# Kernel optimization log

Hardware: AMD Instinct MI355X
Metric: run time of the kernel (lower is better)

Reference implementation:

```python
import jax, jax.numpy as jnp
import numpy as np

B, T, H, NH = 2, 2048, 1024, 16
HD = H // NH


def setup_inputs() -> dict:
    key = jax.random.key(0)
    ks = jax.random.split(key, 12)
    s = 1.0 / np.sqrt(H)
    inp = {
        "q": jax.random.normal(ks[0], (B, T, H), jnp.float32),
        "k": jax.random.normal(ks[1], (B, T, H), jnp.float32),
        "v": jax.random.normal(ks[2], (B, T, H), jnp.float32),
        "mask": jnp.tril(jnp.ones((T, T), jnp.int32))[None, None],  # causal [1,1,T,T]
        "w_q": jax.random.normal(ks[3], (H, H), jnp.float32) * s,
        "b_q": jax.random.normal(ks[4], (H,), jnp.float32) * 0.01,
        "w_k": jax.random.normal(ks[5], (H, H), jnp.float32) * s,
        "b_k": jax.random.normal(ks[6], (H,), jnp.float32) * 0.01,
        "w_v": jax.random.normal(ks[7], (H, H), jnp.float32) * s,
        "b_v": jax.random.normal(ks[8], (H,), jnp.float32) * 0.01,
        "w_o": jax.random.normal(ks[9], (H, H), jnp.float32) * s,
        "b_o": jax.random.normal(ks[10], (H,), jnp.float32) * 0.01,
    }
    return inp


def reference(q, k, v, mask, w_q, b_q, w_k, b_k, w_v, b_v, w_o, b_o):
    def split_heads(x):
        Bx, Tx, _ = x.shape
        return x.reshape(Bx, Tx, NH, HD).transpose(0, 2, 1, 3)  # [B,NH,T,HD]

    Q = split_heads(q @ w_q.T + b_q)
    K = split_heads(k @ w_k.T + b_k)
    V = split_heads(v @ w_v.T + b_v)

    scores = jnp.einsum("bhqd,bhkd->bhqk", Q, K) / np.sqrt(HD).astype(np.float32)
    scores = jnp.where(mask == 0, jnp.float32(-1e9), scores)
    weights = jax.nn.softmax(scores, axis=-1)  # dropout prob = 0.0
    out = jnp.einsum("bhqk,bhkd->bhqd", weights, V)
    out = out.transpose(0, 2, 1, 3).reshape(q.shape[0], q.shape[1], H)
    return out @ w_o.T + b_o
```

## Files before the change

### kernel.cpp

```cpp
#include <hip/hip_runtime.h>
#include <hip/hip_bf16.h>

#define Bb 2
#define Tt 2048
#define Hh 1024
#define NHh 16

typedef short bf16x8 __attribute__((ext_vector_type(8)));
typedef float f32x4 __attribute__((ext_vector_type(4)));
typedef unsigned short u16;
typedef unsigned int u32;
typedef u16 u16x4v __attribute__((ext_vector_type(4)));
typedef u32 u32x2v __attribute__((ext_vector_type(2)));

#define QK_SCALE 0.180336880f

#if __has_builtin(__builtin_amdgcn_exp2f)
__device__ __forceinline__ float exp2_fast(float x) { return __builtin_amdgcn_exp2f(x); }
#else
__device__ __forceinline__ float exp2_fast(float x) { return __expf(x * 0.69314718f); }
#endif

__device__ __forceinline__ u16 f2b(float x) {
  unsigned u = __builtin_bit_cast(unsigned, x);
  u += 0x7FFFu + ((u >> 16) & 1u);
  return (u16)(u >> 16);
}
__device__ __forceinline__ float b2f(u16 x) {
  return __builtin_bit_cast(float, (u32)x << 16);
}

__device__ __forceinline__ u32 cvt_pk(float lo, float hi) {
  u32 r;
  asm("v_cvt_pk_bf16_f32 %0, %1, %2" : "=v"(r) : "v"(lo), "v"(hi));
  return r;
}

__global__ __launch_bounds__(256) void cvt_all_kernel(
    const float* __restrict__ q, const float* __restrict__ k, const float* __restrict__ v,
    const float* __restrict__ wq, const float* __restrict__ wk,
    const float* __restrict__ wv, const float* __restrict__ wo,
    u16* __restrict__ qb, u16* __restrict__ kb, u16* __restrict__ vb,
    u16* __restrict__ wqb, u16* __restrict__ wkb, u16* __restrict__ wvb,
    u16* __restrict__ wob, int n4_in, int n4_w) {
  const int which = blockIdx.y;
  const float* src;
  u16* dst;
  int n4;
  float sc = 1.0f;
  switch (which) {
    case 0: src = q;  dst = qb;  n4 = n4_in; break;
    case 1: src = k;  dst = kb;  n4 = n4_in; break;
    case 2: src = v;  dst = vb;  n4 = n4_in; break;
    case 3: src = wq; dst = wqb; n4 = n4_w; sc = QK_SCALE; break;
    case 4: src = wk; dst = wkb; n4 = n4_w; break;
    case 5: src = wv; dst = wvb; n4 = n4_w; break;
    default: src = wo; dst = wob; n4 = n4_w; break;
  }
  int i = blockIdx.x * blockDim.x + threadIdx.x;
  int stride = gridDim.x * blockDim.x;
  for (; i < n4; i += stride) {
    float4 vv = ((const float4*)src)[i];
    u16x4v o;
    o.x = f2b(vv.x * sc); o.y = f2b(vv.y * sc); o.z = f2b(vv.z * sc); o.w = f2b(vv.w * sc);
    ((u16x4v*)dst)[i] = o;
  }
}

template<int NF, int MODE>
__device__ __forceinline__ void gemm_body(const u16* __restrict__ A,
                                          const u16* __restrict__ W,
                                          const float* __restrict__ bias, float bscale,
                                          void* __restrict__ Cout,
                                          u16* lA, u16* lB, int mt, int nt) {
  const int tid = threadIdx.x;
  const int lane = tid & 63;
  const int wid = tid >> 6;
  const int wr = wid >> 1, wc = wid & 1;
  const int g = lane >> 4, fr = lane & 15;
  constexpr int NT = NF * 32;

  f32x4 acc[4][NF];
#pragma unroll
  for (int m = 0; m < 4; ++m)
#pragma unroll
    for (int n = 0; n < NF; ++n) acc[m][n] = (f32x4){0.f, 0.f, 0.f, 0.f};

  const int srow = tid >> 3;
  const int scol = (tid & 7) * 8;

  bf16x8 ra[4], rb[NF];
#pragma unroll
  for (int ps = 0; ps < 4; ++ps)
    ra[ps] = *(const bf16x8*)(A + (size_t)(mt * 128 + ps * 32 + srow) * Hh + scol);
#pragma unroll
  for (int ps = 0; ps < NF; ++ps)
    rb[ps] = *(const bf16x8*)(W + (size_t)(nt * NT + ps * 32 + srow) * Hh + scol);
#pragma unroll
  for (int ps = 0; ps < 4; ++ps) {
    int r = ps * 32 + srow;
    *(bf16x8*)((char*)lA + r * 128 + ((scol * 2) ^ ((r & 7) << 4))) = ra[ps];
  }
#pragma unroll
  for (int ps = 0; ps < NF; ++ps) {
    int r = ps * 32 + srow;
    *(bf16x8*)((char*)lB + r * 128 + ((scol * 2) ^ ((r & 7) << 4))) = rb[ps];
  }
  __syncthreads();

  for (int kt = 0; kt < Hh; kt += 64) {
    if (kt + 64 < Hh) {
#pragma unroll
      for (int ps = 0; ps < 4; ++ps)
        ra[ps] = *(const bf16x8*)(A + (size_t)(mt * 128 + ps * 32 + srow) * Hh + kt + 64 + scol);
#pragma unroll
      for (int ps = 0; ps < NF; ++ps)
        rb[ps] = *(const bf16x8*)(W + (size_t)(nt * NT + ps * 32 + srow) * Hh + kt + 64 + scol);
    }
    bf16x8 af[4][2], bfv[NF][2];
#pragma unroll
    for (int m = 0; m < 4; ++m)
#pragma unroll
      for (int ks = 0; ks < 2; ++ks) {
        int r = wr * 64 + m * 16 + fr;
        af[m][ks] = *(const bf16x8*)((const char*)lA + r * 128 + ((ks * 64 + g * 16) ^ ((r & 7) << 4)));
      }
#pragma unroll
    for (int n = 0; n < NF; ++n)
#pragma unroll
      for (int ks = 0; ks < 2; ++ks) {
        int r = wc * (NT / 2) + n * 16 + fr;
        bfv[n][ks] = *(const bf16x8*)((const char*)lB + r * 128 + ((ks * 64 + g * 16) ^ ((r & 7) << 4)));
      }
#pragma unroll
    for (int m = 0; m < 4; ++m)
#pragma unroll
      for (int n = 0; n < NF; ++n)
#pragma unroll
        for (int ks = 0; ks < 2; ++ks)
          acc[m][n] = __builtin_amdgcn_mfma_f32_16x16x32_bf16(af[m][ks], bfv[n][ks],
                                                              acc[m][n], 0, 0, 0);
    if (kt + 64 < Hh) {
      __syncthreads();
#pragma unroll
      for (int ps = 0; ps < 4; ++ps) {
        int r = ps * 32 + srow;
        *(bf16x8*)((char*)lA + r * 128 + ((scol * 2) ^ ((r & 7) << 4))) = ra[ps];
      }
#pragma unroll
      for (int ps = 0; ps < NF; ++ps) {
        int r = ps * 32 + srow;
        *(bf16x8*)((char*)lB + r * 128 + ((scol * 2) ^ ((r & 7) << 4))) = rb[ps];
      }
      __syncthreads();
    }
  }

#pragma unroll
  for (int n = 0; n < NF; ++n) {
    int Cc = nt * NT + wc * (NT / 2) + n * 16 + fr;
    float bv = bias[Cc] * bscale;
#pragma unroll
    for (int m = 0; m < 4; ++m) {
#pragma unroll
      for (int j = 0; j < 4; ++j) {
        int R = mt * 128 + wr * 64 + m * 16 + g * 4 + j;
        float val = acc[m][n][j] + bv;
        if constexpr (MODE == 0) {
          int bb = R >> 11, t = R & (Tt - 1);
          int h = Cc >> 6, d = Cc & 63;
          ((u16*)Cout)[(((size_t)(bb * NHh + h) * Tt + t) << 6) + d] = f2b(val);
        } else if constexpr (MODE == 2) {
          int bb = R >> 11, t = R & (Tt - 1);
          int h = Cc >> 6, d = Cc & 63;
          ((u16*)Cout)[(((size_t)(bb * NHh + h) * 64 + d) << 11) + t] = f2b(val);
        } else {
          ((float*)Cout)[(size_t)R * Hh + Cc] = val;
        }
      }
    }
  }
}

__global__ __launch_bounds__(256, 3) void proj_qkv_kernel(
    const u16* __restrict__ qb, const u16* __restrict__ kb, const u16* __restrict__ vb,
    const u16* __restrict__ wqb, const u16* __restrict__ wkb, const u16* __restrict__ wvb,
    const float* __restrict__ biq, const float* __restrict__ bik, const float* __restrict__ biv,
    u16* __restrict__ Qp, u16* __restrict__ Kp, u16* __restrict__ Vt) {
  __shared__ u16 lA[128 * 64];
  __shared__ u16 lB[128 * 64];
  const int id = blockIdx.x;
  const int nt = (id >> 3) & 7;
  const int slot = (id & 7) + 8 * (id >> 6);
  const int z = slot >> 5, mt = slot & 31;
  if (z == 0)      gemm_body<4, 0>(qb, wqb, biq, QK_SCALE, Qp, lA, lB, mt, nt);
  else if (z == 1) gemm_body<4, 0>(kb, wkb, bik, 1.0f, Kp, lA, lB, mt, nt);
  else             gemm_body<4, 2>(vb, wvb, biv, 1.0f, Vt, lA, lB, mt, nt);
}

__global__ __launch_bounds__(256, 2) void gemm_out_kernel(
    const u16* __restrict__ A, const u16* __restrict__ W,
    const float* __restrict__ bias, float* __restrict__ Cout) {
  __shared__ u16 lA[128 * 64];
  __shared__ u16 lB[64 * 64];
  const int id = blockIdx.x;
  const int j = id >> 3;
  const int mt = (id & 7) + 8 * (j >> 4);
  const int nt = j & 15;
  gemm_body<2, 1>(A, W, bias, 1.0f, Cout, lA, lB, mt, nt);
}

__global__ __launch_bounds__(256, 4) void attn_kernel(const u16* __restrict__ Qp,
                                                      const u16* __restrict__ Kp,
                                                      const u16* __restrict__ Vt,
                                                      u16* __restrict__ AO,
                                                      u16* __restrict__ Obuf,
                                                      float2* __restrict__ MLbuf) {
  __shared__ u16 lK[2][64 * 64];
  __shared__ u16 lV[2][64 * 64];
  __shared__ u16 lP[64 * 64];
  const int tid = threadIdx.x;
  const int lane = tid & 63;
  const int w = tid >> 6;
  const int g = lane >> 4, fr = lane & 15;

  const int id = blockIdx.x;
  int bh, qt, kv0, kv1, chunk = 0;
  bool split;
  if (id < 512) {
    bh = id & 31; qt = 16 + (id >> 5);
    kv0 = 0; kv1 = 15; split = true;
  } else {
    int r = id - 512;
    int d = 16 - (r >> 6);
    int p = r & 63;
    bh = p & 31;
    if (p < 32) { qt = d - 1;  kv0 = 0;  kv1 = qt; split = false; }
    else        { qt = 15 + d; kv0 = 16; kv1 = qt; split = true; chunk = 1; }
  }
  const int q0 = qt * 64;

  bf16x8 qf[2];
  {
    const u16* qrow = Qp + (((size_t)bh * Tt + q0 + w * 16 + fr) << 6) + g * 8;
    qf[0] = *(const bf16x8*)(qrow);
    qf[1] = *(const bf16x8*)(qrow + 32);
  }

  const int srow = tid >> 3;
  const int scol = (tid & 7) * 8;
  const int sswz = (scol * 2) ^ ((srow & 7) << 4);

  bf16x8 rk[2], rv[2];
#pragma unroll
  for (int ps = 0; ps < 2; ++ps) {
    rk[ps] = *(const bf16x8*)(Kp + (((size_t)bh * Tt + kv0 * 64 + ps * 32 + srow) << 6) + scol);
    rv[ps] = *(const bf16x8*)(Vt + (((size_t)bh * 64 + ps * 32 + srow) << 11) + kv0 * 64 + scol);
  }
#pragma unroll
  for (int ps = 0; ps < 2; ++ps) {
    *(bf16x8*)((char*)lK[0] + (ps * 32 + srow) * 128 + sswz) = rk[ps];
    *(bf16x8*)((char*)lV[0] + (ps * 32 + srow) * 128 + sswz) = rv[ps];
  }
  __syncthreads();

  float m_r = -1e30f, l_r = 0.f;
  f32x4 acc[4];
#pragma unroll
  for (int nd = 0; nd < 4; ++nd) acc[nd] = (f32x4){0.f, 0.f, 0.f, 0.f};

  const int prow = w * 16 + fr;
  const int psw = (prow & 7) << 4;
  const int qoff = w * 16 + fr;

  for (int jt = kv0; jt <= kv1; ++jt) {
    const char* bK = (const char*)lK[jt & 1];
    const char* bV = (const char*)lV[jt & 1];
    if (jt < kv1) {
#pragma unroll
      for (int ps = 0; ps < 2; ++ps) {
        rk[ps] = *(const bf16x8*)(Kp + (((size_t)bh * Tt + (jt + 1) * 64 + ps * 32 + srow) << 6) + scol);
        rv[ps] = *(const bf16x8*)(Vt + (((size_t)bh * 64 + ps * 32 + srow) << 11) + (jt + 1) * 64 + scol);
      }
    }
    f32x4 s[4];
    __builtin_amdgcn_s_setprio(1);
#pragma unroll
    for (int n = 0; n < 4; ++n) {
      s[n] = (f32x4){0.f, 0.f, 0.f, 0.f};
      int rbase = (n * 16 + fr) * 128;
      int rsw = (fr & 7) << 4;
#pragma unroll
      for (int ks = 0; ks < 2; ++ks) {
        bf16x8 ak = *(const bf16x8*)(bK + rbase + ((ks * 64 + g * 16) ^ rsw));
        s[n] = __builtin_amdgcn_mfma_f32_16x16x32_bf16(ak, qf[ks], s[n], 0, 0, 0);
      }
    }
    __builtin_amdgcn_s_setprio(0);

    float tm = -1e30f;
    if (jt == qt) {
#pragma unroll
      for (int n = 0; n < 4; ++n)
#pragma unroll
        for (int r = 0; r < 4; ++r) {
          if (n * 16 + g * 4 + r > qoff) s[n][r] = -1e30f;
          tm = fmaxf(tm, s[n][r]);
        }
    } else {
#pragma unroll
      for (int n = 0; n < 4; ++n)
#pragma unroll
        for (int r = 0; r < 4; ++r) tm = fmaxf(tm, s[n][r]);
    }
    tm = fmaxf(tm, __shfl_xor(tm, 16));
    tm = fmaxf(tm, __shfl_xor(tm, 32));
    if (!__all(tm <= m_r + 8.0f)) {
      float mn = fmaxf(m_r, tm);
      float sc = exp2_fast(m_r - mn);
      m_r = mn;
      l_r *= sc;
      float scj[4];
#pragma unroll
      for (int j = 0; j < 4; ++j) scj[j] = __shfl(sc, g * 4 + j);
#pragma unroll
      for (int nd = 0; nd < 4; ++nd)
#pragma unroll
        for (int j = 0; j < 4; ++j) acc[nd][j] *= scj[j];
    }
    float rs = 0.f;
    u32 pw[4][2];
#pragma unroll
    for (int n = 0; n < 4; ++n) {
      float p0 = exp2_fast(s[n][0] - m_r);
      float p1 = exp2_fast(s[n][1] - m_r);
      float p2 = exp2_fast(s[n][2] - m_r);
      float p3 = exp2_fast(s[n][3] - m_r);
      rs += (p0 + p1) + (p2 + p3);
      pw[n][0] = cvt_pk(p0, p1);
      pw[n][1] = cvt_pk(p2, p3);
    }
    rs += __shfl_xor(rs, 16);
    rs += __shfl_xor(rs, 32);
    l_r += rs;
    bf16x8 pa[2];
    {
      char* base = (char*)lP + prow * 128;
#pragma unroll
      for (int n = 0; n < 4; ++n)
        *(u32x2v*)(base + ((32 * n + 8 * g) ^ psw)) = (u32x2v){pw[n][0], pw[n][1]};
#pragma unroll
      for (int ks = 0; ks < 2; ++ks)
        pa[ks] = *(const bf16x8*)(base + ((ks * 64 + g * 16) ^ psw));
    }
    __builtin_amdgcn_s_setprio(1);
#pragma unroll
    for (int nd = 0; nd < 4; ++nd) {
      int rbase = (nd * 16 + fr) * 128;
      int rsw = (fr & 7) << 4;
#pragma unroll
      for (int ks = 0; ks < 2; ++ks) {
        bf16x8 bv = *(const bf16x8*)(bV + rbase + ((ks * 64 + g * 16) ^ rsw));
        acc[nd] = __builtin_amdgcn_mfma_f32_16x16x32_bf16(pa[ks], bv, acc[nd], 0, 0, 0);
      }
    }
    __builtin_amdgcn_s_setprio(0);
    if (jt < kv1) {
#pragma unroll
      for (int ps = 0; ps < 2; ++ps) {
        *(bf16x8*)((char*)lK[(jt + 1) & 1] + (ps * 32 + srow) * 128 + sswz) = rk[ps];
        *(bf16x8*)((char*)lV[(jt + 1) & 1] + (ps * 32 + srow) * 128 + sswz) = rv[ps];
      }
      __syncthreads();
    }
  }

  if (!split) {
    const int b = bh >> 4, hh = bh & 15;
    float lj[4];
#pragma unroll
    for (int j = 0; j < 4; ++j) lj[j] = __shfl(l_r, g * 4 + j);
#pragma unroll
    for (int j = 0; j < 4; ++j) {
      float inv = 1.0f / lj[j];
      int qq = q0 + w * 16 + g * 4 + j;
      size_t base = (((size_t)b * Tt + qq) << 10) + hh * 64;
#pragma unroll
      for (int nd = 0; nd < 4; ++nd)
        AO[base + nd * 16 + fr] = f2b(acc[nd][j] * inv);
    }
  } else {
    const int pidx = ((bh * 16 + (qt - 16)) << 1) + chunk;
    if (g == 0) MLbuf[pidx * 64 + w * 16 + fr] = make_float2(m_r, l_r);
    u16* ob = Obuf + (size_t)pidx * 4096;
#pragma unroll
    for (int j = 0; j < 4; ++j) {
      int row = w * 16 + g * 4 + j;
#pragma unroll
      for (int nd = 0; nd < 4; ++nd)
        ob[row * 64 + nd * 16 + fr] = f2b(acc[nd][j]);
    }
  }
}

__global__ __launch_bounds__(256) void merge_kernel(const u16* __restrict__ Obuf,
                                                    const float2* __restrict__ MLbuf,
                                                    u16* __restrict__ AO) {
  const int row_id = blockIdx.x * 256 + threadIdx.x;
  const int bh = row_id >> 10;
  const int qs = (row_id >> 6) & 15;
  const int row = row_id & 63;
  const int tile = bh * 16 + qs;
  float2 ml0 = MLbuf[(tile * 2 + 0) * 64 + row];
  float2 ml1 = MLbuf[(tile * 2 + 1) * 64 + row];
  float M = fmaxf(ml0.x, ml1.x);
  float w0 = exp2_fast(ml0.x - M);
  float w1 = exp2_fast(ml1.x - M);
  float inv = 1.0f / (w0 * ml0.y + w1 * ml1.y);
  const u16* o0 = Obuf + (size_t)(tile * 2 + 0) * 4096 + row * 64;
  const u16* o1 = Obuf + (size_t)(tile * 2 + 1) * 4096 + row * 64;
  const int qt = 16 + qs;
  const int qq = qt * 64 + row;
  const int b = bh >> 4, hh = bh & 15;
  u16* dst = AO + (((size_t)b * Tt + qq) << 10) + hh * 64;
#pragma unroll
  for (int c = 0; c < 8; ++c) {
    bf16x8 v0 = *(const bf16x8*)(o0 + c * 8);
    bf16x8 v1 = *(const bf16x8*)(o1 + c * 8);
    bf16x8 o;
#pragma unroll
    for (int e = 0; e < 8; ++e)
      o[e] = (short)f2b((w0 * b2f((u16)v0[e]) + w1 * b2f((u16)v1[e])) * inv);
    *(bf16x8*)(dst + c * 8) = o;
  }
}

extern "C" void kernel_launch(void* const* d_in, const int* in_sizes, int n_in,
                              void* d_out, int out_size, void* d_ws, size_t ws_size,
                              hipStream_t stream) {
  const float* q   = (const float*)d_in[0];
  const float* k   = (const float*)d_in[1];
  const float* v   = (const float*)d_in[2];
  const float* wq  = (const float*)d_in[4];
  const float* bq  = (const float*)d_in[5];
  const float* wk  = (const float*)d_in[6];
  const float* bk  = (const float*)d_in[7];
  const float* wv  = (const float*)d_in[8];
  const float* bv  = (const float*)d_in[9];
  const float* wo  = (const float*)d_in[10];
  const float* bo  = (const float*)d_in[11];

  char* ws = (char*)d_ws;
  const size_t SZB = (size_t)Bb * Tt * Hh * 2;
  const size_t WB  = (size_t)Hh * Hh * 2;
  u16* qb  = (u16*)(ws);
  u16* kb  = (u16*)(ws + SZB);
  u16* vb  = (u16*)(ws + 2 * SZB);
  u16* wqb = (u16*)(ws + 3 * SZB);
  u16* wkb = (u16*)(ws + 3 * SZB + WB);
  u16* wvb = (u16*)(ws + 3 * SZB + 2 * WB);
  u16* wob = (u16*)(ws + 3 * SZB + 3 * WB);
  u16* Qp  = (u16*)(ws + 3 * SZB + 4 * WB);
  u16* Kp  = (u16*)(ws + 4 * SZB + 4 * WB);
  u16* Vt  = (u16*)(ws + 5 * SZB + 4 * WB);
  u16* AO  = qb;
  u16* Obuf = kb;
  float2* MLbuf = (float2*)vb;

  const int N4_IN = (Bb * Tt * Hh) / 4;
  const int N4_W  = (Hh * Hh) / 4;
  cvt_all_kernel<<<dim3(512, 7), 256, 0, stream>>>(
      q, k, v, wq, wk, wv, wo, qb, kb, vb, wqb, wkb, wvb, wob, N4_IN, N4_W);

  proj_qkv_kernel<<<dim3(768), 256, 0, stream>>>(
      qb, kb, vb, wqb, wkb, wvb, bq, bk, bv, Qp, Kp, Vt);

  attn_kernel<<<dim3(1536), 256, 0, stream>>>(Qp, Kp, Vt, AO, Obuf, MLbuf);

  merge_kernel<<<dim3(128), 256, 0, stream>>>(Obuf, MLbuf, AO);

  gemm_out_kernel<<<dim3(512), 256, 0, stream>>>(
      AO, wob, bo, (float*)d_out);
}
```

Measured before the change: 107.9 us.

## Use 128-row query tiles with 512-thread attention blocks sharing K/V staging

Doubles the attention query tile from 64 to 128 rows by running 8 waves per block, so each K/V tile loaded into LDS serves twice as many queries. The work split, causal mask offsets, split-KV partial buffers and merge kernel indexing are remapped to the new tile size. This halves global K/V traffic per query and the number of staging loads per thread. The cost is larger blocks with more LDS, a coarser grid of 768 blocks, and a causal diagonal that now spans two KV tiles, which adds masking work.

Result: slower. 126.2 us (+17.0%).

```diff
diff --git a/kernel.cpp b/kernel.cpp
--- a/kernel.cpp
+++ b/kernel.cpp
@@ -210,7 +210,7 @@
   gemm_body<2, 1>(A, W, bias, 1.0f, Cout, lA, lB, mt, nt);
 }
 
-__global__ __launch_bounds__(256, 4) void attn_kernel(const u16* __restrict__ Qp,
+__global__ __launch_bounds__(512, 6) void attn_kernel(const u16* __restrict__ Qp,
                                                       const u16* __restrict__ Kp,
                                                       const u16* __restrict__ Vt,
                                                       u16* __restrict__ AO,
@@ -218,27 +218,26 @@
                                                       float2* __restrict__ MLbuf) {
   __shared__ u16 lK[2][64 * 64];
   __shared__ u16 lV[2][64 * 64];
-  __shared__ u16 lP[64 * 64];
+  __shared__ u16 lP[128 * 64];
   const int tid = threadIdx.x;
   const int lane = tid & 63;
   const int w = tid >> 6;
   const int g = lane >> 4, fr = lane & 15;
 
   const int id = blockIdx.x;
-  int bh, qt, kv0, kv1, chunk = 0;
+  const int kk = id >> 8, p = id & 255;
+  const int bh = p >> 3, s = p & 7;
+  int qt, kv0, kv1, chunk = 0;
   bool split;
-  if (id < 512) {
-    bh = id & 31; qt = 16 + (id >> 5);
-    kv0 = 0; kv1 = 15; split = true;
+  if (kk == 0) { qt = 8 + s; kv0 = 0; kv1 = 15; split = true; }
+  else if (kk == 1) {
+    if ((s & 1) == 0) { qt = 7 - (s >> 1); kv0 = 0; kv1 = 2 * qt + 1; split = false; }
+    else { qt = 15 - (s >> 1); kv0 = 16; kv1 = 2 * qt + 1; split = true; chunk = 1; }
   } else {
-    int r = id - 512;
-    int d = 16 - (r >> 6);
-    int p = r & 63;
-    bh = p & 31;
-    if (p < 32) { qt = d - 1;  kv0 = 0;  kv1 = qt; split = false; }
-    else        { qt = 15 + d; kv0 = 16; kv1 = qt; split = true; chunk = 1; }
-  }
-  const int q0 = qt * 64;
+    if ((s & 1) == 0) { qt = (s >> 1); kv0 = 0; kv1 = 2 * qt + 1; split = false; }
+    else { qt = 8 + (s >> 1); kv0 = 16; kv1 = 2 * qt + 1; split = true; chunk = 1; }
+  }
+  const int q0 = qt * 128;
 
   bf16x8 qf[2];
   {
@@ -251,17 +250,11 @@
   const int scol = (tid & 7) * 8;
   const int sswz = (scol * 2) ^ ((srow & 7) << 4);
 
-  bf16x8 rk[2], rv[2];
-#pragma unroll
-  for (int ps = 0; ps < 2; ++ps) {
-    rk[ps] = *(const bf16x8*)(Kp + (((size_t)bh * Tt + kv0 * 64 + ps * 32 + srow) << 6) + scol);
-    rv[ps] = *(const bf16x8*)(Vt + (((size_t)bh * 64 + ps * 32 + srow) << 11) + kv0 * 64 + scol);
-  }
-#pragma unroll
-  for (int ps = 0; ps < 2; ++ps) {
-    *(bf16x8*)((char*)lK[0] + (ps * 32 + srow) * 128 + sswz) = rk[ps];
-    *(bf16x8*)((char*)lV[0] + (ps * 32 + srow) * 128 + sswz) = rv[ps];
-  }
+  bf16x8 rk, rv;
+  rk = *(const bf16x8*)(Kp + (((size_t)bh * Tt + kv0 * 64 + srow) << 6) + scol);
+  rv = *(const bf16x8*)(Vt + (((size_t)bh * 64 + srow) << 11) + kv0 * 64 + scol);
+  *(bf16x8*)((char*)lK[0] + srow * 128 + sswz) = rk;
+  *(bf16x8*)((char*)lV[0] + srow * 128 + sswz) = rv;
   __syncthreads();
 
   float m_r = -1e30f, l_r = 0.f;
@@ -271,47 +264,45 @@
 
   const int prow = w * 16 + fr;
   const int psw = (prow & 7) << 4;
-  const int qoff = w * 16 + fr;
+  const int qrow = w * 16 + fr;
 
   for (int jt = kv0; jt <= kv1; ++jt) {
     const char* bK = (const char*)lK[jt & 1];
     const char* bV = (const char*)lV[jt & 1];
     if (jt < kv1) {
-#pragma unroll
-      for (int ps = 0; ps < 2; ++ps) {
-        rk[ps] = *(const bf16x8*)(Kp + (((size_t)bh * Tt + (jt + 1) * 64 + ps * 32 + srow) << 6) + scol);
-        rv[ps] = *(const bf16x8*)(Vt + (((size_t)bh * 64 + ps * 32 + srow) << 11) + (jt + 1) * 64 + scol);
-      }
-    }
-    f32x4 s[4];
+      rk = *(const bf16x8*)(Kp + (((size_t)bh * Tt + (jt + 1) * 64 + srow) << 6) + scol);
+      rv = *(const bf16x8*)(Vt + (((size_t)bh * 64 + srow) << 11) + (jt + 1) * 64 + scol);
+    }
+    f32x4 sv4[4];
     __builtin_amdgcn_s_setprio(1);
 #pragma unroll
     for (int n = 0; n < 4; ++n) {
-      s[n] = (f32x4){0.f, 0.f, 0.f, 0.f};
+      sv4[n] = (f32x4){0.f, 0.f, 0.f, 0.f};
       int rbase = (n * 16 + fr) * 128;
       int rsw = (fr & 7) << 4;
 #pragma unroll
       for (int ks = 0; ks < 2; ++ks) {
         bf16x8 ak = *(const bf16x8*)(bK + rbase + ((ks * 64 + g * 16) ^ rsw));
-        s[n] = __builtin_amdgcn_mfma_f32_16x16x32_bf16(ak, qf[ks], s[n], 0, 0, 0);
+        sv4[n] = __builtin_amdgcn_mfma_f32_16x16x32_bf16(ak, qf[ks], sv4[n], 0, 0, 0);
       }
     }
     __builtin_amdgcn_s_setprio(0);
 
     float tm = -1e30f;
-    if (jt == qt) {
+    if (jt >= 2 * qt) {
+      const int dj = (jt - 2 * qt) << 6;
 #pragma unroll
       for (int n = 0; n < 4; ++n)
 #pragma unroll
         for (int r = 0; r < 4; ++r) {
-          if (n * 16 + g * 4 + r > qoff) s[n][r] = -1e30f;
-          tm = fmaxf(tm, s[n][r]);
+          if (dj + n * 16 + g * 4 + r > qrow) sv4[n][r] = -1e30f;
+          tm = fmaxf(tm, sv4[n][r]);
         }
     } else {
 #pragma unroll
       for (int n = 0; n < 4; ++n)
 #pragma unroll
-        for (int r = 0; r < 4; ++r) tm = fmaxf(tm, s[n][r]);
+        for (int r = 0; r < 4; ++r) tm = fmaxf(tm, sv4[n][r]);
     }
     tm = fmaxf(tm, __shfl_xor(tm, 16));
     tm = fmaxf(tm, __shfl_xor(tm, 32));
@@ -332,10 +323,10 @@
     u32 pw[4][2];
 #pragma unroll
     for (int n = 0; n < 4; ++n) {
-      float p0 = exp2_fast(s[n][0] - m_r);
-      float p1 = exp2_fast(s[n][1] - m_r);
-      float p2 = exp2_fast(s[n][2] - m_r);
-      float p3 = exp2_fast(s[n][3] - m_r);
+      float p0 = exp2_fast(sv4[n][0] - m_r);
+      float p1 = exp2_fast(sv4[n][1] - m_r);
+      float p2 = exp2_fast(sv4[n][2] - m_r);
+      float p3 = exp2_fast(sv4[n][3] - m_r);
       rs += (p0 + p1) + (p2 + p3);
       pw[n][0] = cvt_pk(p0, p1);
       pw[n][1] = cvt_pk(p2, p3);
@@ -366,11 +357,8 @@
     }
     __builtin_amdgcn_s_setprio(0);
     if (jt < kv1) {
-#pragma unroll
-      for (int ps = 0; ps < 2; ++ps) {
-        *(bf16x8*)((char*)lK[(jt + 1) & 1] + (ps * 32 + srow) * 128 + sswz) = rk[ps];
-        *(bf16x8*)((char*)lV[(jt + 1) & 1] + (ps * 32 + srow) * 128 + sswz) = rv[ps];
-      }
+      *(bf16x8*)((char*)lK[(jt + 1) & 1] + srow * 128 + sswz) = rk;
+      *(bf16x8*)((char*)lV[(jt + 1) & 1] + srow * 128 + sswz) = rv;
       __syncthreads();
     }
   }
@@ -390,9 +378,9 @@
         AO[base + nd * 16 + fr] = f2b(acc[nd][j] * inv);
     }
   } else {
-    const int pidx = ((bh * 16 + (qt - 16)) << 1) + chunk;
-    if (g == 0) MLbuf[pidx * 64 + w * 16 + fr] = make_float2(m_r, l_r);
-    u16* ob = Obuf + (size_t)pidx * 4096;
+    const int pidx = ((bh * 8 + (qt - 8)) << 1) + chunk;
+    if (g == 0) MLbuf[pidx * 128 + w * 16 + fr] = make_float2(m_r, l_r);
+    u16* ob = Obuf + (size_t)pidx * 8192;
 #pragma unroll
     for (int j = 0; j < 4; ++j) {
       int row = w * 16 + g * 4 + j;
@@ -408,19 +396,19 @@
                                                     u16* __restrict__ AO) {
   const int row_id = blockIdx.x * 256 + threadIdx.x;
   const int bh = row_id >> 10;
-  const int qs = (row_id >> 6) & 15;
-  const int row = row_id & 63;
-  const int tile = bh * 16 + qs;
-  float2 ml0 = MLbuf[(tile * 2 + 0) * 64 + row];
-  float2 ml1 = MLbuf[(tile * 2 + 1) * 64 + row];
+  const int qs = (row_id >> 7) & 7;
+  const int row = row_id & 127;
+  const int tile = bh * 8 + qs;
+  float2 ml0 = MLbuf[(tile * 2 + 0) * 128 + row];
+  float2 ml1 = MLbuf[(tile * 2 + 1) * 128 + row];
   float M = fmaxf(ml0.x, ml1.x);
   float w0 = exp2_fast(ml0.x - M);
   float w1 = exp2_fast(ml1.x - M);
   float inv = 1.0f / (w0 * ml0.y + w1 * ml1.y);
-  const u16* o0 = Obuf + (size_t)(tile * 2 + 0) * 4096 + row * 64;
-  const u16* o1 = Obuf + (size_t)(tile * 2 + 1) * 4096 + row * 64;
-  const int qt = 16 + qs;
-  const int qq = qt * 64 + row;
+  const u16* o0 = Obuf + (size_t)(tile * 2 + 0) * 8192 + row * 64;
+  const u16* o1 = Obuf + (size_t)(tile * 2 + 1) * 8192 + row * 64;
+  const int qt = 8 + qs;
+  const int qq = qt * 128 + row;
   const int b = bh >> 4, hh = bh & 15;
   u16* dst = AO + (((size_t)b * Tt + qq) << 10) + hh * 64;
 #pragma unroll
@@ -475,7 +463,7 @@
   proj_qkv_kernel<<<dim3(768), 256, 0, stream>>>(
       qb, kb, vb, wqb, wkb, wvb, bq, bk, bv, Qp, Kp, Vt);
 
-  attn_kernel<<<dim3(1536), 256, 0, stream>>>(Qp, Kp, Vt, AO, Obuf, MLbuf);
+  attn_kernel<<<dim3(768), 512, 0, stream>>>(Qp, Kp, Vt, AO, Obuf, MLbuf);
 
   merge_kernel<<<dim3(128), 256, 0, stream>>>(Obuf, MLbuf, AO);
 
```
